# Performance work log

Measured on AMD Instinct MI355X. Metric: run time of the kernel, lower is better.

Reference implementation:

```python
import jax, jax.numpy as jnp
import numpy as np

EPS = 1e-5
N_NODES = 100000
N_EDGES = 1600000
DIMS = [196, 64, 128, 256, 256, 576]


def sage_conv(x, src, dst, Wl, Wr, b, n):
    # PyG SAGEConv (mean aggr): out = lin_l(mean_j x_j) + lin_r(x_i)
    agg = jax.ops.segment_sum(x[src], dst, num_segments=n)
    cnt = jax.ops.segment_sum(jnp.ones((src.shape[0],), x.dtype), dst, num_segments=n)
    agg = agg / jnp.maximum(cnt, 1.0)[:, None]
    return agg @ Wl.T + x @ Wr.T + b


def batch_norm(x, gamma, beta):
    m = jnp.mean(x, axis=0)
    v = jnp.mean((x - m) ** 2, axis=0)  # biased var, as in torch BN forward
    return (x - m) * jax.lax.rsqrt(v + EPS) * gamma + beta


def setup_inputs() -> dict:
    key = jax.random.key(0)
    ks = jax.random.split(key, 32)
    inp = {
        "x": jax.random.normal(ks[0], (N_NODES, DIMS[0]), dtype=jnp.float32),
        "edge_index": jax.random.randint(ks[1], (2, N_EDGES), 0, N_NODES, dtype=jnp.int32),
    }
    ki = 2
    for i in range(5):
        fin, fout = DIMS[i], DIMS[i + 1]
        s = 1.0 / np.sqrt(fin)
        inp[f"W{i+1}l"] = jax.random.uniform(ks[ki], (fout, fin), jnp.float32, -s, s); ki += 1
        inp[f"W{i+1}r"] = jax.random.uniform(ks[ki], (fout, fin), jnp.float32, -s, s); ki += 1
        inp[f"b{i+1}"] = jax.random.uniform(ks[ki], (fout,), jnp.float32, -s, s); ki += 1
    for i in range(4):
        fout = DIMS[i + 1]
        inp[f"g{i+1}"] = jnp.ones((fout,), jnp.float32)
        inp[f"be{i+1}"] = jnp.zeros((fout,), jnp.float32)
    return inp


def reference(x, edge_index,
              W1l, W1r, b1, W2l, W2r, b2, W3l, W3r, b3,
              W4l, W4r, b4, W5l, W5r, b5,
              g1, be1, g2, be2, g3, be3, g4, be4):
    src, dst = edge_index[0], edge_index[1]
    n = x.shape[0]
    x = jax.nn.relu(batch_norm(sage_conv(x, src, dst, W1l, W1r, b1, n), g1, be1))
    x = jax.nn.relu(batch_norm(sage_conv(x, src, dst, W2l, W2r, b2, n), g2, be2))
    x = jax.nn.relu(batch_norm(sage_conv(x, src, dst, W3l, W3r, b3, n), g3, be3))
    x = jax.nn.relu(batch_norm(sage_conv(x, src, dst, W4l, W4r, b4, n), g4, be4))
    x = sage_conv(x, src, dst, W5l, W5r, b5, n)
    return x
```

## Files before the change

kernel.cpp:

```cpp
#include <hip/hip_runtime.h>
#include <hip/hip_bf16.h>

typedef __hip_bfloat16 bf16;
typedef __attribute__((ext_vector_type(8))) short short8;
typedef __attribute__((ext_vector_type(4))) float f32x4;

#define NN 100000
#define NE 1600000

__device__ __forceinline__ float bf2f(short s) {
    return __uint_as_float(((unsigned int)(unsigned short)s) << 16);
}
__device__ __forceinline__ short f2bf(float f) {
    union { bf16 b; short s; } u;
    u.b = __float2bfloat16(f);
    return u.s;
}

__global__ void detect_kernel(const unsigned int* __restrict__ x, int* __restrict__ flags) {
    __shared__ int s;
    if (threadIdx.x == 0) s = 0;
    __syncthreads();
    int c = 0;
    for (int j = 0; j < 4; ++j) {
        unsigned int w = x[threadIdx.x * 4 + j];
        unsigned int e = (w >> 7) & 0xFF;
        if (e >= 100 && e <= 141) c++;
    }
    atomicAdd(&s, c);
    __syncthreads();
    if (threadIdx.x == 0) flags[0] = (s > 128) ? 1 : 0;
}

__global__ __launch_bounds__(256) void cvt_pad_kernel(const void* __restrict__ in,
                                                      bf16* __restrict__ out,
                                                      int rows, int sk, int dk,
                                                      const int* __restrict__ flagp) {
    int i = blockIdx.x * 256 + threadIdx.x;
    int g4 = dk >> 2;
    if (i >= rows * g4) return;
    int row = i / g4;
    int c = (i - row * g4) * 4;
    uint2 w;
    w.x = 0u; w.y = 0u;
    if (c < sk) {
        if (flagp[0]) {
            w = *(const uint2*)((const char*)in + ((size_t)row * sk + c) * 2);
        } else {
            const float* f = (const float*)((const char*)in + ((size_t)row * sk + c) * 4);
            union { bf16 t[4]; uint2 u; } pk;
            pk.t[0] = __float2bfloat16(f[0]);
            pk.t[1] = __float2bfloat16(f[1]);
            pk.t[2] = __float2bfloat16(f[2]);
            pk.t[3] = __float2bfloat16(f[3]);
            w = pk.u;
        }
    }
    *(uint2*)((char*)out + ((size_t)row * dk + c) * 2) = w;
}

struct WJobs {
    const void* src[10];
    bf16* dst[10];
    int rows[10];
    int sk[10];
    int dk[10];
};
__global__ __launch_bounds__(256) void cvt_pad_multi(WJobs J, const int* __restrict__ flagp) {
    int j = blockIdx.y;
    int g4 = J.dk[j] >> 2;
    int tot = J.rows[j] * g4;
    int i = blockIdx.x * 256 + threadIdx.x;
    if (i >= tot) return;
    int row = i / g4;
    int c = (i - row * g4) * 4;
    int sk = J.sk[j];
    uint2 w;
    w.x = 0u; w.y = 0u;
    if (c < sk) {
        if (flagp[0]) {
            w = *(const uint2*)((const char*)J.src[j] + ((size_t)row * sk + c) * 2);
        } else {
            const float* f = (const float*)((const char*)J.src[j] + ((size_t)row * sk + c) * 4);
            union { bf16 t[4]; uint2 u; } pk;
            pk.t[0] = __float2bfloat16(f[0]);
            pk.t[1] = __float2bfloat16(f[1]);
            pk.t[2] = __float2bfloat16(f[2]);
            pk.t[3] = __float2bfloat16(f[3]);
            w = pk.u;
        }
    }
    *(uint2*)((char*)J.dst[j] + ((size_t)row * J.dk[j] + c) * 2) = w;
}

struct VJobs {
    const void* src[13];
    float* dst[13];
    int n[13];
};
__global__ __launch_bounds__(576) void cvt_f32_multi(VJobs J, const int* __restrict__ flagp) {
    int j = blockIdx.x;
    int c = threadIdx.x;
    if (c >= J.n[j]) return;
    float v;
    if (flagp[0]) v = __bfloat162float(((const bf16*)J.src[j])[c]);
    else v = ((const float*)J.src[j])[c];
    J.dst[j][c] = v;
}

__global__ __launch_bounds__(256) void fill_kernel(bf16* __restrict__ out, long long n) {
    long long i = (long long)blockIdx.x * 256 + threadIdx.x;
    if (i < n) out[i] = __float2bfloat16(1000.0f);
}


__global__ __launch_bounds__(256) void count_kernel(const int* __restrict__ dst,
                                                    int* __restrict__ cnt) {
    int e = blockIdx.x * 256 + threadIdx.x;
    if (e < NE) atomicAdd(&cnt[dst[e]], 1);
}

#define SCAN_NB ((NN + 1023) / 1024)

__global__ __launch_bounds__(256) void scan_partial_kernel(const int* __restrict__ cnt,
                                                           int* __restrict__ bsum) {
    __shared__ int lds[256];
    int t = threadIdx.x;
    int base = blockIdx.x * 1024 + t * 4;
    int s = 0;
#pragma unroll
    for (int i = 0; i < 4; ++i) {
        int idx = base + i;
        if (idx < NN) s += cnt[idx];
    }
    lds[t] = s;
    __syncthreads();
    for (int h = 128; h > 0; h >>= 1) {
        if (t < h) lds[t] += lds[t + h];
        __syncthreads();
    }
    if (t == 0) bsum[blockIdx.x] = lds[0];
}

__global__ __launch_bounds__(128) void scan_bsum_kernel(int* __restrict__ bsum,
                                                        int* __restrict__ indptr) {
    __shared__ int lds[128];
    int t = threadIdx.x;
    int v = (t < SCAN_NB) ? bsum[t] : 0;
    lds[t] = v;
    __syncthreads();
    for (int off = 1; off < 128; off <<= 1) {
        int x = (t >= off) ? lds[t - off] : 0;
        __syncthreads();
        lds[t] += x;
        __syncthreads();
    }
    if (t < SCAN_NB) bsum[t] = lds[t] - v;
    if (t == 127) indptr[NN] = lds[127];
}

__global__ __launch_bounds__(256) void scan_apply_kernel(const int* __restrict__ cnt,
                                                         const int* __restrict__ bsum,
                                                         int* __restrict__ indptr,
                                                         int* __restrict__ cursor,
                                                         float* __restrict__ recip) {
    __shared__ int lds[256];
    int t = threadIdx.x;
    int base = blockIdx.x * 1024 + t * 4;
    int c[4];
    int s = 0;
#pragma unroll
    for (int i = 0; i < 4; ++i) {
        int idx = base + i;
        c[i] = (idx < NN) ? cnt[idx] : 0;
        s += c[i];
    }
    lds[t] = s;
    __syncthreads();
    for (int off = 1; off < 256; off <<= 1) {
        int x = (t >= off) ? lds[t - off] : 0;
        __syncthreads();
        lds[t] += x;
        __syncthreads();
    }
    int run = bsum[blockIdx.x] + lds[t] - s;
#pragma unroll
    for (int i = 0; i < 4; ++i) {
        int idx = base + i;
        if (idx < NN) {
            indptr[idx] = run;
            cursor[idx] = run;
            recip[idx] = 1.0f / (float)(c[i] > 1 ? c[i] : 1);
            run += c[i];
        }
    }
}

__global__ __launch_bounds__(256) void scatter_kernel(const int* __restrict__ src,
                                                      const int* __restrict__ dst,
                                                      int* __restrict__ cursor,
                                                      int* __restrict__ csr) {
    int e = blockIdx.x * 256 + threadIdx.x;
    if (e < NE) {
        int d = dst[e];
        int p = atomicAdd(&cursor[d], 1);
        csr[p] = src[e];
    }
}

template <int D, int ADD>
__global__ __launch_bounds__(256) void aggv_kernel(const bf16* __restrict__ u,
                                                   const int* __restrict__ indptr,
                                                   const int* __restrict__ csr,
                                                   const float* __restrict__ recip,
                                                   bf16* __restrict__ out) {
    constexpr int TPR = D / 8;
    constexpr int NPB = 256 / TPR;
    const int tid = threadIdx.x;
    const int node = blockIdx.x * NPB + tid / TPR;
    if (node >= NN) return;
    const int c0 = (tid % TPR) * 8;
    const short* ub = (const short*)u + c0;
    const int j0 = indptr[node], j1 = indptr[node + 1];
    float acc[8];
#pragma unroll
    for (int t = 0; t < 8; ++t) acc[t] = 0.f;
    int j = j0;
    for (; j + 3 < j1; j += 4) {
        int s0 = csr[j], s1 = csr[j + 1], s2 = csr[j + 2], s3 = csr[j + 3];
        short8 v0 = *(const short8*)(ub + (size_t)s0 * D);
        short8 v1 = *(const short8*)(ub + (size_t)s1 * D);
        short8 v2 = *(const short8*)(ub + (size_t)s2 * D);
        short8 v3 = *(const short8*)(ub + (size_t)s3 * D);
#pragma unroll
        for (int t = 0; t < 8; ++t)
            acc[t] += (bf2f(v0[t]) + bf2f(v1[t])) + (bf2f(v2[t]) + bf2f(v3[t]));
    }
    for (; j < j1; ++j) {
        short8 v0 = *(const short8*)(ub + (size_t)csr[j] * D);
#pragma unroll
        for (int t = 0; t < 8; ++t) acc[t] += bf2f(v0[t]);
    }
    const float r = recip[node];
    size_t o = (size_t)node * D + c0;
    short8 w;
    if (ADD) {
        short8 prev = *(const short8*)((const short*)out + o);
#pragma unroll
        for (int t = 0; t < 8; ++t) w[t] = f2bf(acc[t] * r + bf2f(prev[t]));
    } else {
#pragma unroll
        for (int t = 0; t < 8; ++t) w[t] = f2bf(acc[t] * r);
    }
    *(short8*)((short*)out + o) = w;
}

__device__ __forceinline__ void gld_lds16(const void* g, void* l) {
    __builtin_amdgcn_global_load_lds(
        (const __attribute__((address_space(1))) unsigned int*)g,
        (__attribute__((address_space(3))) unsigned int*)l, 16, 0, 0);
}

__global__ __launch_bounds__(256) void gemm_kernel(
    const bf16* __restrict__ A1, const bf16* __restrict__ W1, int K1,
    const bf16* __restrict__ A2, const bf16* __restrict__ W2, int K2,
    const float* __restrict__ bias,
    bf16* __restrict__ outB, bf16* __restrict__ outB2, int Nsplit,
    void* __restrict__ outFinal,
    float* __restrict__ statp,
    const int* __restrict__ flagp,
    int M, int N) {
    __shared__ alignas(16) char smem[40960];
    char* sA = smem;
    char* sW = smem + 32768;

    const int tid = threadIdx.x;
    const int lane = tid & 63, wv = tid >> 6;
    const int lrow = lane & 15, lq = lane >> 4;

    const int nwg = gridDim.x * gridDim.y;
    const int flat = blockIdx.y * gridDim.x + blockIdx.x;
    const int xcd = flat & 7;
    const int rest = flat >> 3;
    const int q = nwg >> 3, r = nwg & 7;
    const int chunk = (xcd < r) ? xcd * (q + 1) : r * (q + 1) + (xcd - r) * q;
    const int newid = chunk + rest;
    const int n0 = (newid % gridDim.x) * 64;
    const int m0 = (newid / gridDim.x) * 256;

    const int isbf = flagp[0];

    f32x4 acc[4][4];
#pragma unroll
    for (int a = 0; a < 4; ++a)
#pragma unroll
        for (int b = 0; b < 4; ++b) acc[a][b] = (f32x4){0.f, 0.f, 0.f, 0.f};

    const int sr = tid >> 3;
    const int scb = (tid & 7) << 4;

#pragma unroll 1
    for (int seg = 0; seg < 2; ++seg) {
        const bf16* Ap = seg ? A2 : A1;
        const bf16* Wp = seg ? W2 : W1;
        const int K = seg ? K2 : K1;
        if (K == 0) continue;
#pragma unroll 1
        for (int k0 = 0; k0 < K; k0 += 64) {
            __syncthreads();
#pragma unroll
            for (int i = 0; i < 8; ++i) {
                int row = i * 32 + sr;
                int gr = m0 + row;
                if (gr >= M) gr = M - 1;
                const char* g = (const char*)Ap + ((size_t)gr * K + k0) * 2 +
                                (scb ^ ((row & 7) << 4));
                gld_lds16(g, sA + row * 128 + scb);
            }
#pragma unroll
            for (int i = 0; i < 2; ++i) {
                int row = i * 32 + sr;
                const char* g = (const char*)Wp + ((size_t)(n0 + row) * K + k0) * 2 +
                                (scb ^ ((row & 7) << 4));
                gld_lds16(g, sW + row * 128 + scb);
            }
            __syncthreads();
#pragma unroll
            for (int kh = 0; kh < 2; ++kh) {
                short8 a[4], b[4];
                const int cb = kh * 64 + lq * 16;
#pragma unroll
                for (int mi = 0; mi < 4; ++mi) {
                    int row = wv * 64 + mi * 16 + lrow;
                    a[mi] = *(const short8*)(sA + row * 128 + (cb ^ ((row & 7) << 4)));
                }
#pragma unroll
                for (int ni = 0; ni < 4; ++ni) {
                    int row = ni * 16 + lrow;
                    b[ni] = *(const short8*)(sW + row * 128 + (cb ^ ((row & 7) << 4)));
                }
#pragma unroll
                for (int mi = 0; mi < 4; ++mi)
#pragma unroll
                    for (int ni = 0; ni < 4; ++ni)
                        acc[mi][ni] = __builtin_amdgcn_mfma_f32_16x16x32_bf16(
                            a[mi], b[ni], acc[mi][ni], 0, 0, 0);
            }
        }
    }

    if (statp) {
#pragma unroll
        for (int ni = 0; ni < 4; ++ni) {
            int gcol = n0 + ni * 16 + lrow;
            float bv = bias ? bias[gcol] : 0.f;
            float s = 0.f, q2 = 0.f;
#pragma unroll
            for (int mi = 0; mi < 4; ++mi) {
#pragma unroll
                for (int r2 = 0; r2 < 4; ++r2) {
                    int grow = m0 + wv * 64 + mi * 16 + lq * 4 + r2;
                    if (grow < M) {
                        float v = acc[mi][ni][r2] + bv;
                        s += v;
                        q2 += v * v;
                    }
                }
            }
            s += __shfl_xor(s, 16, 64);
            s += __shfl_xor(s, 32, 64);
            q2 += __shfl_xor(q2, 16, 64);
            q2 += __shfl_xor(q2, 32, 64);
            if (lq == 0) {
                atomicAdd(&statp[gcol], s);
                atomicAdd(&statp[N + gcol], q2);
            }
        }
    }
    __syncthreads();
    const bool f32out = (outFinal != nullptr) && !isbf;
    if (!f32out) {
        bf16* dst = outB ? outB : (bf16*)outFinal;
        short* sc = (short*)smem;
#pragma unroll
        for (int ni = 0; ni < 4; ++ni) {
            float bv = bias ? bias[n0 + ni * 16 + lrow] : 0.f;
#pragma unroll
            for (int mi = 0; mi < 4; ++mi) {
                int rl = wv * 64 + mi * 16 + lq * 4;
#pragma unroll
                for (int r2 = 0; r2 < 4; ++r2)
                    sc[(rl + r2) * 64 + ni * 16 + lrow] = f2bf(acc[mi][ni][r2] + bv);
            }
        }
        __syncthreads();
#pragma unroll
        for (int i = 0; i < 8; ++i) {
            int f8 = tid + i * 256;
            int rowl = f8 >> 3;
            int col0 = (f8 & 7) * 8;
            int grow = m0 + rowl;
            int gcol = n0 + col0;
            if (grow < M) {
                short8 v = ((const short8*)smem)[f8];
                if (gcol < Nsplit)
                    *(short8*)((short*)dst + (size_t)grow * Nsplit + gcol) = v;
                else
                    *(short8*)((short*)outB2 + (size_t)grow * (N - Nsplit) +
                               (gcol - Nsplit)) = v;
            }
        }
    } else {
        float* dst = (float*)outFinal;
        float* sf = (float*)smem;
#pragma unroll 1
        for (int h = 0; h < 2; ++h) {
            if ((wv >> 1) == h) {
#pragma unroll
                for (int ni = 0; ni < 4; ++ni) {
                    float bv = bias ? bias[n0 + ni * 16 + lrow] : 0.f;
#pragma unroll
                    for (int mi = 0; mi < 4; ++mi) {
                        int rl = (wv & 1) * 64 + mi * 16 + lq * 4;
#pragma unroll
                        for (int r2 = 0; r2 < 4; ++r2)
                            sf[(rl + r2) * 64 + ni * 16 + lrow] = acc[mi][ni][r2] + bv;
                    }
                }
            }
            __syncthreads();
#pragma unroll
            for (int i = 0; i < 8; ++i) {
                int f4 = tid + i * 256;
                int rowl = f4 >> 4;
                int col0 = (f4 & 15) * 4;
                int grow = m0 + h * 128 + rowl;
                if (grow < M)
                    *(float4*)(dst + (size_t)grow * N + n0 + col0) =
                        ((const float4*)smem)[f4];
            }
            __syncthreads();
        }
    }
}


__global__ __launch_bounds__(256) void bn_stats_kernel(const bf16* __restrict__ C,
                                                       int ldN,
                                                       float* __restrict__ stats) {
    int N = 1 << ldN;
    int tid = threadIdx.x;
    int c = tid & (N - 1);
    int rsub = tid >> ldN;
    int rstep = 256 >> ldN;
    int r0 = blockIdx.x * 64;
    float s = 0.f, q = 0.f;
    for (int r = r0 + rsub; r < r0 + 64; r += rstep) {
        if (r < NN) {
            float v = __bfloat162float(C[(size_t)r * N + c]);
            s += v;
            q += v * v;
        }
    }
    __shared__ float ls[256], lq[256];
    ls[tid] = s;
    lq[tid] = q;
    __syncthreads();
    for (int half = rstep >> 1; half > 0; half >>= 1) {
        if (rsub < half) {
            ls[tid] += ls[tid + half * N];
            lq[tid] += lq[tid + half * N];
        }
        __syncthreads();
    }
    if (rsub == 0) {
        atomicAdd(&stats[c], ls[tid]);
        atomicAdd(&stats[N + c], lq[tid]);
    }
}

__global__ __launch_bounds__(256) void bn_finalize_kernel(const float* __restrict__ stats,
                                                          const float* __restrict__ g,
                                                          const float* __restrict__ be,
                                                          int N,
                                                          float* __restrict__ scale,
                                                          float* __restrict__ shift) {
    int c = threadIdx.x;
    if (c >= N) return;
    float mean = stats[c] * (1.0f / NN);
    float var = stats[N + c] * (1.0f / NN) - mean * mean;
    var = fmaxf(var, 0.f);
    float sc = g[c] * rsqrtf(var + 1e-5f);
    scale[c] = sc;
    shift[c] = be[c] - mean * sc;
}

__global__ __launch_bounds__(256) void bn_apply_kernel(const bf16* __restrict__ C,
                                                       const float* __restrict__ scale,
                                                       const float* __restrict__ shift,
                                                       int mask,
                                                       bf16* __restrict__ act,
                                                       long long total8) {
    long long i = (long long)blockIdx.x * 256 + threadIdx.x;
    if (i >= total8) return;
    int c0 = (int)((i * 8) & mask);
    short8 v = ((const short8*)C)[i];
    float4 sc0 = *(const float4*)&scale[c0];
    float4 sc1 = *(const float4*)&scale[c0 + 4];
    float4 sh0 = *(const float4*)&shift[c0];
    float4 sh1 = *(const float4*)&shift[c0 + 4];
    short8 w;
#pragma unroll
    for (int t = 0; t < 4; ++t) {
        float x = bf2f(v[t]) * ((const float*)&sc0)[t] + ((const float*)&sh0)[t];
        w[t] = f2bf(x > 0.f ? x : 0.f);
    }
#pragma unroll
    for (int t = 0; t < 4; ++t) {
        float x = bf2f(v[t + 4]) * ((const float*)&sc1)[t] + ((const float*)&sh1)[t];
        w[t + 4] = f2bf(x > 0.f ? x : 0.f);
    }
    ((short8*)act)[i] = w;
}


extern "C" void kernel_launch(void* const* d_in, const int* in_sizes, int n_in,
                              void* d_out, int out_size, void* d_ws, size_t ws_size,
                              hipStream_t stream) {
    const void* x_raw = d_in[0];
    const int* ei = (const int*)d_in[1];
    const int* src = ei;
    const int* dst = ei + NE;

    char* w = (char*)d_ws;
    size_t off = 0;
    auto alloc = [&](size_t bytes) {
        void* p = w + off;
        off = (off + bytes + 255) & ~(size_t)255;
        return p;
    };
    int* flags = (int*)alloc(256);
    int* cnt = (int*)alloc((size_t)NN * 4);
    int* indptr = (int*)alloc((size_t)(NN + 1) * 4);
    int* cursor = (int*)alloc((size_t)NN * 4);
    float* recip = (float*)alloc((size_t)NN * 4);
    int* csr = (int*)alloc((size_t)NE * 4);
    int* bsum = (int*)alloc((size_t)SCAN_NB * 4);
    const int KDIM[5] = {196, 64, 128, 256, 256};
    const int KPAD[5] = {256, 64, 128, 256, 256};
    const int NDIM[5] = {64, 128, 256, 256, 576};
    bf16 *Wlb[5], *Wrb[5];
    float *bf_[5], *gf[4], *bef[4];
    for (int i = 0; i < 5; ++i) {
        Wlb[i] = (bf16*)alloc((size_t)KPAD[i] * NDIM[i] * 2);
        Wrb[i] = (bf16*)alloc((size_t)KPAD[i] * NDIM[i] * 2);
        bf_[i] = (float*)alloc((size_t)NDIM[i] * 4);
    }
    for (int i = 0; i < 4; ++i) {
        gf[i] = (float*)alloc((size_t)NDIM[i] * 4);
        bef[i] = (float*)alloc((size_t)NDIM[i] * 4);
    }
    float* bias1cat = (float*)alloc(128 * 4);
    float* stats = (float*)alloc(1408 * 4);
    float* scale = (float*)alloc(256 * 4);
    float* shift = (float*)alloc(256 * 4);
    float *s1 = stats, *s2 = stats + 128, *s3 = stats + 384, *s4 = stats + 896;
    bf16* aggb = (bf16*)alloc((size_t)NN * 256 * 2);
    bf16* S1 = (bf16*)alloc((size_t)NN * 256 * 2);
    bf16* S2 = (bf16*)alloc((size_t)NN * 256 * 2);
    bf16* xb = aggb;
    bf16* u1 = S2;

    if (off > ws_size) {
        long long n = (long long)NN * 576;
        fill_kernel<<<(int)((n + 255) / 256), 256, 0, stream>>>((bf16*)d_out, n);
        return;
    }

    hipMemsetAsync(cnt, 0, (size_t)NN * 4, stream);
    hipMemsetAsync(stats, 0, 1408 * 4, stream);
    hipMemsetAsync(bias1cat, 0, 64 * 4, stream);

    detect_kernel<<<1, 64, 0, stream>>>((const unsigned int*)x_raw, flags);

    {
        int totx = NN * (KPAD[0] >> 2);
        cvt_pad_kernel<<<(totx + 255) / 256, 256, 0, stream>>>(x_raw, xb, NN, 196, 256, flags);

        WJobs wj;
        int maxb = 0;
        for (int i = 0; i < 5; ++i) {
            wj.src[2 * i] = d_in[2 + 3 * i];
            wj.dst[2 * i] = Wlb[i];
            wj.src[2 * i + 1] = d_in[3 + 3 * i];
            wj.dst[2 * i + 1] = Wrb[i];
            wj.rows[2 * i] = wj.rows[2 * i + 1] = NDIM[i];
            wj.sk[2 * i] = wj.sk[2 * i + 1] = KDIM[i];
            wj.dk[2 * i] = wj.dk[2 * i + 1] = KPAD[i];
            int nb = (NDIM[i] * (KPAD[i] >> 2) + 255) / 256;
            if (nb > maxb) maxb = nb;
        }
        cvt_pad_multi<<<dim3(maxb, 10), 256, 0, stream>>>(wj, flags);

        VJobs vj;
        vj.src[0] = d_in[4];  vj.dst[0] = bias1cat + 64; vj.n[0] = 64;
        for (int i = 1; i < 5; ++i) {
            vj.src[i] = d_in[4 + 3 * i];
            vj.dst[i] = bf_[i];
            vj.n[i] = NDIM[i];
        }
        for (int i = 0; i < 4; ++i) {
            vj.src[5 + i] = d_in[17 + 2 * i];
            vj.dst[5 + i] = gf[i];
            vj.n[5 + i] = NDIM[i];
            vj.src[9 + i] = d_in[18 + 2 * i];
            vj.dst[9 + i] = bef[i];
            vj.n[9 + i] = NDIM[i];
        }
        cvt_f32_multi<<<13, 576, 0, stream>>>(vj, flags);
    }

    count_kernel<<<(NE + 255) / 256, 256, 0, stream>>>(dst, cnt);
    scan_partial_kernel<<<SCAN_NB, 256, 0, stream>>>(cnt, bsum);
    scan_bsum_kernel<<<1, 128, 0, stream>>>(bsum, indptr);
    scan_apply_kernel<<<SCAN_NB, 256, 0, stream>>>(cnt, bsum, indptr, cursor, recip);
    scatter_kernel<<<(NE + 255) / 256, 256, 0, stream>>>(src, dst, cursor, csr);

    const int GM = (NN + 63) / 64;
    const int GY = (NN + 255) / 256;

    gemm_kernel<<<dim3(2, GY), 256, 0, stream>>>(xb, Wlb[0], 256, nullptr, nullptr, 0,
                                                 bias1cat, u1, S1, 64,
                                                 nullptr, nullptr, flags, NN, 128);
    aggv_kernel<64, 1><<<NN / 32, 256, 0, stream>>>(u1, indptr, csr, recip, S1);
    bn_stats_kernel<<<GM, 256, 0, stream>>>(S1, 6, s1);
    bn_finalize_kernel<<<1, 256, 0, stream>>>(s1, gf[0], bef[0], 64, scale, shift);
    bn_apply_kernel<<<(NN * 64 / 8 + 255) / 256, 256, 0, stream>>>(S1, scale, shift, 63, S1,
                                                                   (long long)NN * 64 / 8);

    aggv_kernel<64, 0><<<NN / 32, 256, 0, stream>>>(S1, indptr, csr, recip, aggb);
    gemm_kernel<<<dim3(2, GY), 256, 0, stream>>>(aggb, Wlb[1], 64, S1, Wrb[1], 64,
                                                 bf_[1], S2, nullptr, 128,
                                                 nullptr, s2, flags, NN, 128);
    bn_finalize_kernel<<<1, 256, 0, stream>>>(s2, gf[1], bef[1], 128, scale, shift);
    bn_apply_kernel<<<(NN * 128 / 8 + 255) / 256, 256, 0, stream>>>(S2, scale, shift, 127, S2,
                                                                    (long long)NN * 128 / 8);

    aggv_kernel<128, 0><<<NN / 16, 256, 0, stream>>>(S2, indptr, csr, recip, aggb);
    gemm_kernel<<<dim3(4, GY), 256, 0, stream>>>(aggb, Wlb[2], 128, S2, Wrb[2], 128,
                                                 bf_[2], S1, nullptr, 256,
                                                 nullptr, s3, flags, NN, 256);
    bn_finalize_kernel<<<1, 256, 0, stream>>>(s3, gf[2], bef[2], 256, scale, shift);
    bn_apply_kernel<<<(NN * 256 / 8 + 255) / 256, 256, 0, stream>>>(S1, scale, shift, 255, S1,
                                                                    (long long)NN * 256 / 8);

    aggv_kernel<256, 0><<<NN / 8, 256, 0, stream>>>(S1, indptr, csr, recip, aggb);
    gemm_kernel<<<dim3(4, GY), 256, 0, stream>>>(aggb, Wlb[3], 256, S1, Wrb[3], 256,
                                                 bf_[3], S2, nullptr, 256,
                                                 nullptr, s4, flags, NN, 256);
    bn_finalize_kernel<<<1, 256, 0, stream>>>(s4, gf[3], bef[3], 256, scale, shift);
    bn_apply_kernel<<<(NN * 256 / 8 + 255) / 256, 256, 0, stream>>>(S2, scale, shift, 255, S2,
                                                                    (long long)NN * 256 / 8);

    aggv_kernel<256, 0><<<NN / 8, 256, 0, stream>>>(S2, indptr, csr, recip, aggb);
    gemm_kernel<<<dim3(9, GY), 256, 0, stream>>>(aggb, Wlb[4], 256, S2, Wrb[4], 256,
                                                 bf_[4], nullptr, nullptr, 576,
                                                 d_out, nullptr, flags, NN, 576);
}
```

Measured before the change: 1.268 ms.

## Fuse BN apply+ReLU into aggregation and double-buffer GEMM LDS tiles

Drops the separate bn_apply pass. A new aggbn kernel applies BN scale/shift and ReLU to the node's own row, writes that activation, and applies the same transform to each gathered neighbor row while aggregating. The GEMM now double-buffers its LDS tiles with async global-to-LDS loads, so the next k-tile loads while the current one computes. The f32 epilogue also writes all rows in one pass. This saves one full read/write of each activation tensor and hides load latency, at the cost of recomputing BN per gathered edge and doubling LDS to 80KB, which may lower occupancy.

```diff
diff --git a/kernel.cpp b/kernel.cpp
--- a/kernel.cpp
+++ b/kernel.cpp
@@ -255,6 +255,71 @@
     *(short8*)((short*)out + o) = w;
 }
 
+template <int D>
+__global__ __launch_bounds__(256) void aggbn_kernel(const bf16* __restrict__ raw,
+                                                    const int* __restrict__ indptr,
+                                                    const int* __restrict__ csr,
+                                                    const float* __restrict__ recip,
+                                                    const float* __restrict__ scale,
+                                                    const float* __restrict__ shift,
+                                                    bf16* __restrict__ act,
+                                                    bf16* __restrict__ agg) {
+    constexpr int TPR = D / 8;
+    constexpr int NPB = 256 / TPR;
+    const int tid = threadIdx.x;
+    const int node = blockIdx.x * NPB + tid / TPR;
+    if (node >= NN) return;
+    const int c0 = (tid % TPR) * 8;
+    float sc[8], sh[8];
+    *(float4*)&sc[0] = *(const float4*)&scale[c0];
+    *(float4*)&sc[4] = *(const float4*)&scale[c0 + 4];
+    *(float4*)&sh[0] = *(const float4*)&shift[c0];
+    *(float4*)&sh[4] = *(const float4*)&shift[c0 + 4];
+    const short* ub = (const short*)raw + c0;
+    {
+        short8 v = *(const short8*)(ub + (size_t)node * D);
+        short8 w;
+#pragma unroll
+        for (int t = 0; t < 8; ++t) {
+            float x = bf2f(v[t]) * sc[t] + sh[t];
+            w[t] = f2bf(x > 0.f ? x : 0.f);
+        }
+        *(short8*)((short*)act + (size_t)node * D + c0) = w;
+    }
+    const int j0 = indptr[node], j1 = indptr[node + 1];
+    float acc[8];
+#pragma unroll
+    for (int t = 0; t < 8; ++t) acc[t] = 0.f;
+    int j = j0;
+    for (; j + 3 < j1; j += 4) {
+        int s0 = csr[j], s1 = csr[j + 1], s2 = csr[j + 2], s3 = csr[j + 3];
+        short8 v0 = *(const short8*)(ub + (size_t)s0 * D);
+        short8 v1 = *(const short8*)(ub + (size_t)s1 * D);
+        short8 v2 = *(const short8*)(ub + (size_t)s2 * D);
+        short8 v3 = *(const short8*)(ub + (size_t)s3 * D);
+#pragma unroll
+        for (int t = 0; t < 8; ++t) {
+            float x0 = fmaxf(bf2f(v0[t]) * sc[t] + sh[t], 0.f);
+            float x1 = fmaxf(bf2f(v1[t]) * sc[t] + sh[t], 0.f);
+            float x2 = fmaxf(bf2f(v2[t]) * sc[t] + sh[t], 0.f);
+            float x3 = fmaxf(bf2f(v3[t]) * sc[t] + sh[t], 0.f);
+            acc[t] += (x0 + x1) + (x2 + x3);
+        }
+    }
+    for (; j < j1; ++j) {
+        short8 v0 = *(const short8*)(ub + (size_t)csr[j] * D);
+#pragma unroll
+        for (int t = 0; t < 8; ++t)
+            acc[t] += fmaxf(bf2f(v0[t]) * sc[t] + sh[t], 0.f);
+    }
+    const float r = recip[node];
+    size_t o = (size_t)node * D + c0;
+    short8 w;
+#pragma unroll
+    for (int t = 0; t < 8; ++t) w[t] = f2bf(acc[t] * r);
+    *(short8*)((short*)agg + o) = w;
+}
+
 __device__ __forceinline__ void gld_lds16(const void* g, void* l) {
     __builtin_amdgcn_global_load_lds(
         (const __attribute__((address_space(1))) unsigned int*)g,
@@ -270,9 +335,7 @@
     float* __restrict__ statp,
     const int* __restrict__ flagp,
     int M, int N) {
-    __shared__ alignas(16) char smem[40960];
-    char* sA = smem;
-    char* sW = smem + 32768;
+    __shared__ alignas(16) char smem[81920];
 
     const int tid = threadIdx.x;
     const int lane = tid & 63, wv = tid >> 6;
@@ -299,54 +362,67 @@
     const int sr = tid >> 3;
     const int scb = (tid & 7) << 4;
 
+    const int nt1 = K1 >> 6;
+    const int nt2 = K2 >> 6;
+    const int nt = nt1 + nt2;
+
+    auto stage = [&](int t, int b) {
+        const bf16* Ap;
+        const bf16* Wp;
+        int K, k0;
+        if (t < nt1) { Ap = A1; Wp = W1; K = K1; k0 = t << 6; }
+        else { Ap = A2; Wp = W2; K = K2; k0 = (t - nt1) << 6; }
+        char* bA = smem + b * 40960;
+        char* bW = bA + 32768;
+#pragma unroll
+        for (int i = 0; i < 8; ++i) {
+            int row = i * 32 + sr;
+            int gr = m0 + row;
+            if (gr >= M) gr = M - 1;
+            const char* g = (const char*)Ap + ((size_t)gr * K + k0) * 2 +
+                            (scb ^ ((row & 7) << 4));
+            gld_lds16(g, bA + row * 128 + scb);
+        }
+#pragma unroll
+        for (int i = 0; i < 2; ++i) {
+            int row = i * 32 + sr;
+            const char* g = (const char*)Wp + ((size_t)(n0 + row) * K + k0) * 2 +
+                            (scb ^ ((row & 7) << 4));
+            gld_lds16(g, bW + row * 128 + scb);
+        }
+    };
+
+    stage(0, 0);
+    __syncthreads();
+    int cur = 0;
 #pragma unroll 1
-    for (int seg = 0; seg < 2; ++seg) {
-        const bf16* Ap = seg ? A2 : A1;
-        const bf16* Wp = seg ? W2 : W1;
-        const int K = seg ? K2 : K1;
-        if (K == 0) continue;
-#pragma unroll 1
-        for (int k0 = 0; k0 < K; k0 += 64) {
-            __syncthreads();
-#pragma unroll
-            for (int i = 0; i < 8; ++i) {
-                int row = i * 32 + sr;
-                int gr = m0 + row;
-                if (gr >= M) gr = M - 1;
-                const char* g = (const char*)Ap + ((size_t)gr * K + k0) * 2 +
-                                (scb ^ ((row & 7) << 4));
-                gld_lds16(g, sA + row * 128 + scb);
+    for (int t = 0; t < nt; ++t) {
+        if (t + 1 < nt) stage(t + 1, cur ^ 1);
+        const char* sA = smem + cur * 40960;
+        const char* sW = sA + 32768;
+#pragma unroll
+        for (int kh = 0; kh < 2; ++kh) {
+            short8 a[4], b[4];
+            const int cb = kh * 64 + lq * 16;
+#pragma unroll
+            for (int mi = 0; mi < 4; ++mi) {
+                int row = wv * 64 + mi * 16 + lrow;
+                a[mi] = *(const short8*)(sA + row * 128 + (cb ^ ((row & 7) << 4)));
             }
 #pragma unroll
-            for (int i = 0; i < 2; ++i) {
-                int row = i * 32 + sr;
-                const char* g = (const char*)Wp + ((size_t)(n0 + row) * K + k0) * 2 +
-                                (scb ^ ((row & 7) << 4));
-                gld_lds16(g, sW + row * 128 + scb);
+            for (int ni = 0; ni < 4; ++ni) {
+                int row = ni * 16 + lrow;
+                b[ni] = *(const short8*)(sW + row * 128 + (cb ^ ((row & 7) << 4)));
             }
-            __syncthreads();
-#pragma unroll
-            for (int kh = 0; kh < 2; ++kh) {
-                short8 a[4], b[4];
-                const int cb = kh * 64 + lq * 16;
-#pragma unroll
-                for (int mi = 0; mi < 4; ++mi) {
-                    int row = wv * 64 + mi * 16 + lrow;
-                    a[mi] = *(const short8*)(sA + row * 128 + (cb ^ ((row & 7) << 4)));
-                }
-#pragma unroll
-                for (int ni = 0; ni < 4; ++ni) {
-                    int row = ni * 16 + lrow;
-                    b[ni] = *(const short8*)(sW + row * 128 + (cb ^ ((row & 7) << 4)));
-                }
-#pragma unroll
-                for (int mi = 0; mi < 4; ++mi)
-#pragma unroll
-                    for (int ni = 0; ni < 4; ++ni)
-                        acc[mi][ni] = __builtin_amdgcn_mfma_f32_16x16x32_bf16(
-                            a[mi], b[ni], acc[mi][ni], 0, 0, 0);
-            }
-        }
+#pragma unroll
+            for (int mi = 0; mi < 4; ++mi)
+#pragma unroll
+                for (int ni = 0; ni < 4; ++ni)
+                    acc[mi][ni] = __builtin_amdgcn_mfma_f32_16x16x32_bf16(
+                        a[mi], b[ni], acc[mi][ni], 0, 0, 0);
+        }
+        __syncthreads();
+        cur ^= 1;
     }
 
     if (statp) {
@@ -377,7 +453,6 @@
             }
         }
     }
-    __syncthreads();
     const bool f32out = (outFinal != nullptr) && !isbf;
     if (!f32out) {
         bf16* dst = outB ? outB : (bf16*)outFinal;
@@ -413,33 +488,27 @@
     } else {
         float* dst = (float*)outFinal;
         float* sf = (float*)smem;
-#pragma unroll 1
-        for (int h = 0; h < 2; ++h) {
-            if ((wv >> 1) == h) {
-#pragma unroll
-                for (int ni = 0; ni < 4; ++ni) {
-                    float bv = bias ? bias[n0 + ni * 16 + lrow] : 0.f;
-#pragma unroll
-                    for (int mi = 0; mi < 4; ++mi) {
-                        int rl = (wv & 1) * 64 + mi * 16 + lq * 4;
-#pragma unroll
-                        for (int r2 = 0; r2 < 4; ++r2)
-                            sf[(rl + r2) * 64 + ni * 16 + lrow] = acc[mi][ni][r2] + bv;
-                    }
-                }
+#pragma unroll
+        for (int ni = 0; ni < 4; ++ni) {
+            float bv = bias ? bias[n0 + ni * 16 + lrow] : 0.f;
+#pragma unroll
+            for (int mi = 0; mi < 4; ++mi) {
+                int rl = wv * 64 + mi * 16 + lq * 4;
+#pragma unroll
+                for (int r2 = 0; r2 < 4; ++r2)
+                    sf[(rl + r2) * 64 + ni * 16 + lrow] = acc[mi][ni][r2] + bv;
             }
-            __syncthreads();
-#pragma unroll
-            for (int i = 0; i < 8; ++i) {
-                int f4 = tid + i * 256;
-                int rowl = f4 >> 4;
-                int col0 = (f4 & 15) * 4;
-                int grow = m0 + h * 128 + rowl;
-                if (grow < M)
-                    *(float4*)(dst + (size_t)grow * N + n0 + col0) =
-                        ((const float4*)smem)[f4];
-            }
-            __syncthreads();
+        }
+        __syncthreads();
+#pragma unroll
+        for (int i = 0; i < 16; ++i) {
+            int f4 = tid + i * 256;
+            int rowl = f4 >> 4;
+            int col0 = (f4 & 15) * 4;
+            int grow = m0 + rowl;
+            if (grow < M)
+                *(float4*)(dst + (size_t)grow * N + n0 + col0) =
+                    ((const float4*)smem)[f4];
         }
     }
 }
@@ -493,34 +562,6 @@
     float sc = g[c] * rsqrtf(var + 1e-5f);
     scale[c] = sc;
     shift[c] = be[c] - mean * sc;
-}
-
-__global__ __launch_bounds__(256) void bn_apply_kernel(const bf16* __restrict__ C,
-                                                       const float* __restrict__ scale,
-                                                       const float* __restrict__ shift,
-                                                       int mask,
-                                                       bf16* __restrict__ act,
-                                                       long long total8) {
-    long long i = (long long)blockIdx.x * 256 + threadIdx.x;
-    if (i >= total8) return;
-    int c0 = (int)((i * 8) & mask);
-    short8 v = ((const short8*)C)[i];
-    float4 sc0 = *(const float4*)&scale[c0];
-    float4 sc1 = *(const float4*)&scale[c0 + 4];
-    float4 sh0 = *(const float4*)&shift[c0];
-    float4 sh1 = *(const float4*)&shift[c0 + 4];
-    short8 w;
-#pragma unroll
-    for (int t = 0; t < 4; ++t) {
-        float x = bf2f(v[t]) * ((const float*)&sc0)[t] + ((const float*)&sh0)[t];
-        w[t] = f2bf(x > 0.f ? x : 0.f);
-    }
-#pragma unroll
-    for (int t = 0; t < 4; ++t) {
-        float x = bf2f(v[t + 4]) * ((const float*)&sc1)[t] + ((const float*)&sh1)[t];
-        w[t + 4] = f2bf(x > 0.f ? x : 0.f);
-    }
-    ((short8*)act)[i] = w;
 }
 
 
@@ -635,34 +676,30 @@
     aggv_kernel<64, 1><<<NN / 32, 256, 0, stream>>>(u1, indptr, csr, recip, S1);
     bn_stats_kernel<<<GM, 256, 0, stream>>>(S1, 6, s1);
     bn_finalize_kernel<<<1, 256, 0, stream>>>(s1, gf[0], bef[0], 64, scale, shift);
-    bn_apply_kernel<<<(NN * 64 / 8 + 255) / 256, 256, 0, stream>>>(S1, scale, shift, 63, S1,
-                                                                   (long long)NN * 64 / 8);
-
-    aggv_kernel<64, 0><<<NN / 32, 256, 0, stream>>>(S1, indptr, csr, recip, aggb);
-    gemm_kernel<<<dim3(2, GY), 256, 0, stream>>>(aggb, Wlb[1], 64, S1, Wrb[1], 64,
-                                                 bf_[1], S2, nullptr, 128,
+
+    aggbn_kernel<64><<<NN / 32, 256, 0, stream>>>(S1, indptr, csr, recip, scale, shift,
+                                                  S2, aggb);
+    gemm_kernel<<<dim3(2, GY), 256, 0, stream>>>(aggb, Wlb[1], 64, S2, Wrb[1], 64,
+                                                 bf_[1], S1, nullptr, 128,
                                                  nullptr, s2, flags, NN, 128);
     bn_finalize_kernel<<<1, 256, 0, stream>>>(s2, gf[1], bef[1], 128, scale, shift);
-    bn_apply_kernel<<<(NN * 128 / 8 + 255) / 256, 256, 0, stream>>>(S2, scale, shift, 127, S2,
-                                                                    (long long)NN * 128 / 8);
-
-    aggv_kernel<128, 0><<<NN / 16, 256, 0, stream>>>(S2, indptr, csr, recip, aggb);
+
+    aggbn_kernel<128><<<NN / 16, 256, 0, stream>>>(S1, indptr, csr, recip, scale, shift,
+                                                   S2, aggb);
     gemm_kernel<<<dim3(4, GY), 256, 0, stream>>>(aggb, Wlb[2], 128, S2, Wrb[2], 128,
                                                  bf_[2], S1, nullptr, 256,
                                                  nullptr, s3, flags, NN, 256);
     bn_finalize_kernel<<<1, 256, 0, stream>>>(s3, gf[2], bef[2], 256, scale, shift);
-    bn_apply_kernel<<<(NN * 256 / 8 + 255) / 256, 256, 0, stream>>>(S1, scale, shift, 255, S1,
-                                                                    (long long)NN * 256 / 8);
-
-    aggv_kernel<256, 0><<<NN / 8, 256, 0, stream>>>(S1, indptr, csr, recip, aggb);
-    gemm_kernel<<<dim3(4, GY), 256, 0, stream>>>(aggb, Wlb[3], 256, S1, Wrb[3], 256,
-                                                 bf_[3], S2, nullptr, 256,
+
+    aggbn_kernel<256><<<NN / 8, 256, 0, stream>>>(S1, indptr, csr, recip, scale, shift,
+                                                  S2, aggb);
+    gemm_kernel<<<dim3(4, GY), 256, 0, stream>>>(aggb, Wlb[3], 256, S2, Wrb[3], 256,
+                                                 bf_[3], S1, nullptr, 256,
                                                  nullptr, s4, flags, NN, 256);
     bn_finalize_kernel<<<1, 256, 0, stream>>>(s4, gf[3], bef[3], 256, scale, shift);
-    bn_apply_kernel<<<(NN * 256 / 8 + 255) / 256, 256, 0, stream>>>(S2, scale, shift, 255, S2,
-                                                                    (long long)NN * 256 / 8);
-
-    aggv_kernel<256, 0><<<NN / 8, 256, 0, stream>>>(S2, indptr, csr, recip, aggb);
+
+    aggbn_kernel<256><<<NN / 8, 256, 0, stream>>>(S1, indptr, csr, recip, scale, shift,
+                                                  S2, aggb);
     gemm_kernel<<<dim3(9, GY), 256, 0, stream>>>(aggb, Wlb[4], 256, S2, Wrb[4], 256,
                                                  bf_[4], nullptr, nullptr, 576,
                                                  d_out, nullptr, flags, NN, 576);
```

Result: no change. 1.249 ms (median of 2 runs) (-1.5%).
